# Kernel optimization log

Hardware: AMD Instinct MI355X
Metric: run time of the kernel (lower is better)

Reference implementation:

```python
import jax, jax.numpy as jnp
import numpy as np

NUM_HEADS = 32
NUM_KV_HEADS = 8
HEAD_DIM = 64
HIDDEN = 2048
EPS = 1e-05
ROPE_THETA = 1000000.0


def _rmsnorm(x, w):
    # x: [..., head_dim]
    var = jnp.mean(x * x, axis=-1, keepdims=True)
    return w * (x * jax.lax.rsqrt(var + EPS))


def _rope(q, k):
    # q,k: [B, h, T, d]
    T, d = q.shape[2], q.shape[3]
    inv_freq = 1.0 / (ROPE_THETA ** (jnp.arange(0, d, 2, dtype=jnp.float32) / d))
    t = jnp.arange(T, dtype=jnp.float32)
    freqs = jnp.outer(t, inv_freq)               # [T, d/2]
    emb = jnp.concatenate([freqs, freqs], -1)    # [T, d]
    cos = jnp.cos(emb)[None, None].astype(q.dtype)
    sin = jnp.sin(emb)[None, None].astype(q.dtype)

    def rotate(x):
        x1, x2 = x[..., : d // 2], x[..., d // 2 :]
        return jnp.concatenate([-x2, x1], -1)

    return q * cos + rotate(q) * sin, k * cos + rotate(k) * sin


def setup_inputs() -> dict:
    key = jax.random.key(0)
    ks = jax.random.split(key, 7)
    s = 0.02
    x = jax.random.normal(ks[0], (2, 2048, HIDDEN), jnp.float32)
    Wq = jax.random.normal(ks[1], (HIDDEN, NUM_HEADS * HEAD_DIM), jnp.float32) * s
    Wk = jax.random.normal(ks[2], (HIDDEN, NUM_KV_HEADS * HEAD_DIM), jnp.float32) * s
    Wv = jax.random.normal(ks[3], (HIDDEN, NUM_KV_HEADS * HEAD_DIM), jnp.float32) * s
    Wo = jax.random.normal(ks[4], (NUM_HEADS * HEAD_DIM, HIDDEN), jnp.float32) * s
    q_ln_w = jnp.ones((HEAD_DIM,), jnp.float32)
    k_ln_w = jnp.ones((HEAD_DIM,), jnp.float32)
    return {"x": x, "Wq": Wq, "Wk": Wk, "Wv": Wv, "Wo": Wo, "q_ln_w": q_ln_w, "k_ln_w": k_ln_w}


def reference(x, Wq, Wk, Wv, Wo, q_ln_w, k_ln_w):
    B, T, _ = x.shape
    g = NUM_HEADS // NUM_KV_HEADS  # GQA groups = 4
    q = (x @ Wq).reshape(B, T, NUM_HEADS, HEAD_DIM)
    k = (x @ Wk).reshape(B, T, NUM_KV_HEADS, HEAD_DIM)
    v = (x @ Wv).reshape(B, T, NUM_KV_HEADS, HEAD_DIM)
    q = _rmsnorm(q, q_ln_w)
    k = _rmsnorm(k, k_ln_w)
    q = q.transpose(0, 2, 1, 3)  # [B, nh, T, d]
    k = k.transpose(0, 2, 1, 3)  # [B, nkv, T, d]
    v = v.transpose(0, 2, 1, 3)
    q, k = _rope(q, k)
    # native GQA: fold query heads into (kv_head, group) without repeating K/V
    qg = q.reshape(B, NUM_KV_HEADS, g, T, HEAD_DIM)
    scale = 1.0 / jnp.sqrt(jnp.array(HEAD_DIM, q.dtype))
    scores = jnp.einsum("bkgtd,bksd->bkgts", qg, k) * scale  # [B,nkv,g,T,T]
    causal = jnp.tril(jnp.ones((T, T), bool))
    scores = jnp.where(causal, scores, jnp.finfo(scores.dtype).min)
    probs = jax.nn.softmax(scores, axis=-1)
    out = jnp.einsum("bkgts,bksd->bkgtd", probs, v)  # [B,nkv,g,T,d]
    out = out.reshape(B, NUM_HEADS, T, HEAD_DIM).transpose(0, 2, 1, 3).reshape(B, T, -1)
    return out @ Wo
```

## Files before the change

### kernel.cpp

```cpp
#include <hip/hip_runtime.h>
#include <cstdint>
#include <cstddef>

typedef unsigned short u16;
typedef __attribute__((ext_vector_type(8))) short short8;
typedef __attribute__((ext_vector_type(4))) short short4v;
typedef __attribute__((ext_vector_type(4))) float float4v;
typedef __attribute__((ext_vector_type(4))) unsigned short ushort4v;
typedef __attribute__((ext_vector_type(2))) float float2v;

__device__ __forceinline__ u16 f2bf(float f) {
    union { float f; uint32_t u; } x; x.f = f;
    uint32_t r = x.u + 0x7fffu + ((x.u >> 16) & 1u);
    return (u16)(r >> 16);
}
__device__ __forceinline__ uint32_t pack_bf16x2(float lo, float hi) {
    union { float f; uint32_t u; } a, b; a.f = lo; b.f = hi;
    return __builtin_amdgcn_perm(b.u + 0x8000u, a.u + 0x8000u, 0x07060302u);
}
__device__ __forceinline__ void gl_lds16(const u16* g, u16* l) {
    __builtin_amdgcn_global_load_lds(
        (const __attribute__((address_space(1))) void*)g,
        (__attribute__((address_space(3))) void*)l, 16, 0, 0);
}

__global__ __launch_bounds__(256) void prep(const float4v* __restrict__ x,
                                            const float* __restrict__ Wq,
                                            const float* __restrict__ Wk,
                                            const float* __restrict__ Wv,
                                            const float* __restrict__ Wo,
                                            ushort4v* __restrict__ xb,
                                            u16* __restrict__ wqkv_t,
                                            u16* __restrict__ wo_t,
                                            float2v* __restrict__ tab) {
    __shared__ float lds[64][33];
    const int bid = blockIdx.x;
    const int tid = threadIdx.x;
    if (bid < 8192) {
        const int i = bid * 256 + tid;
        float4v v = x[i];
        ushort4v o;
        #pragma unroll
        for (int j = 0; j < 4; ++j) o[j] = f2bf(v[j]);
        xb[i] = o;
        return;
    }
    if (bid < 8448) {
        const int idx = (bid - 8192) * 256 + tid;
        const int t = idx >> 5;
        const int i = idx & 31;
        const float invf = exp2f(-(float)i * (19.931568569324174f / 32.0f));
        float sv, cv;
        sincosf((float)t * invf, &sv, &cv);
        float2v o; o[0] = cv; o[1] = sv;
        tab[idx] = o;
        return;
    }
    const float* src;
    int Ns, n0, k0, scol0;
    u16* dst;
    if (bid < 11520) {
        const int id = bid - 8448;
        const int bx = id % 96, by = id / 96;
        n0 = bx * 32; k0 = by * 64;
        if (n0 < 2048)      { src = Wq; Ns = 2048; scol0 = n0; }
        else if (n0 < 2560) { src = Wk; Ns = 512;  scol0 = n0 - 2048; }
        else                { src = Wv; Ns = 512;  scol0 = n0 - 2560; }
        dst = wqkv_t;
    } else {
        const int id = bid - 11520;
        const int bx = id & 63, by = id >> 6;
        n0 = bx * 32; k0 = by * 64;
        src = Wo; Ns = 2048; scol0 = n0;
        dst = wo_t;
    }
    const int row64 = tid >> 2;
    const int c8    = (tid & 3) * 8;
    const float* sp = src + (size_t)(k0 + row64) * Ns + scol0 + c8;
    const float4v va = *(const float4v*)sp;
    const float4v vb = *(const float4v*)(sp + 4);
    #pragma unroll
    for (int i = 0; i < 4; ++i) { lds[row64][c8 + i] = va[i]; lds[row64][c8 + 4 + i] = vb[i]; }
    __syncthreads();
    const int nrow = tid >> 3;
    const int kk   = (tid & 7) * 8;
    short8 o8;
    #pragma unroll
    for (int i = 0; i < 8; ++i) o8[i] = (short)f2bf(lds[kk + i][nrow]);
    *(short8*)(dst + (size_t)(n0 + nrow) * 2048 + k0 + kk) = o8;
}

__global__ __launch_bounds__(256, 3) void gemm_bt(const u16* __restrict__ A,
                                                  const u16* __restrict__ Bt,
                                                  float* __restrict__ C,
                                                  int M, int N, int K) {
    __shared__ u16 lds_a[128 * 32];
    __shared__ u16 lds_b[128 * 32];
    const int tid  = threadIdx.x;
    const int wave = tid >> 6;
    const int lane = tid & 63;
    const int quad = lane >> 4;
    const int l15  = lane & 15;
    const long m0 = (long)blockIdx.x * 128;
    const long n0 = (long)blockIdx.y * 128;
    const int wm = (wave >> 1) * 64;
    const int wn = (wave & 1) * 64;
    const int s_row = tid >> 2;
    const int s_col = (tid & 3) * 8;

    float4v acc[4][4];
    #pragma unroll
    for (int i = 0; i < 4; ++i)
        #pragma unroll
        for (int j = 0; j < 4; ++j)
            #pragma unroll
            for (int r = 0; r < 4; ++r) acc[i][j][r] = 0.0f;

    const u16* ga0 = A  + (m0 + s_row) * (long)K + s_col;
    const u16* ga1 = ga0 + 64 * (long)K;
    const u16* gb0 = Bt + (n0 + s_row) * (long)K + s_col;
    const u16* gb1 = gb0 + 64 * (long)K;
    u16* la = lds_a + tid * 8;
    u16* lb = lds_b + tid * 8;

    const int n_k = K >> 5;
    for (int it = 0; it < n_k; ++it) {
        const int k0 = it << 5;
        gl_lds16(ga0 + k0, la);
        gl_lds16(ga1 + k0, la + 2048);
        gl_lds16(gb0 + k0, lb);
        gl_lds16(gb1 + k0, lb + 2048);
        __syncthreads();
        short8 af[4], bfr[4];
        #pragma unroll
        for (int mt = 0; mt < 4; ++mt)
            af[mt] = *(const short8*)(lds_a + (wm + mt * 16 + l15) * 32 + quad * 8);
        #pragma unroll
        for (int nt = 0; nt < 4; ++nt)
            bfr[nt] = *(const short8*)(lds_b + (wn + nt * 16 + l15) * 32 + quad * 8);
        #pragma unroll
        for (int mt = 0; mt < 4; ++mt)
            #pragma unroll
            for (int nt = 0; nt < 4; ++nt)
                acc[mt][nt] = __builtin_amdgcn_mfma_f32_16x16x32_bf16(af[mt], bfr[nt], acc[mt][nt], 0, 0, 0);
        __syncthreads();
    }
    #pragma unroll
    for (int mt = 0; mt < 4; ++mt) {
        #pragma unroll
        for (int nt = 0; nt < 4; ++nt) {
            const long gr = m0 + wm + mt * 16 + quad * 4;
            const long gc = n0 + wn + nt * 16 + l15;
            #pragma unroll
            for (int r = 0; r < 4; ++r)
                C[(gr + r) * N + gc] = acc[mt][nt][r];
        }
    }
}

__global__ __launch_bounds__(256, 3) void gemm_qkv(const u16* __restrict__ A,
                                                   const u16* __restrict__ Bt,
                                                   const float* __restrict__ qw,
                                                   const float* __restrict__ kw,
                                                   const float2v* __restrict__ tab,
                                                   u16* __restrict__ Qr,
                                                   u16* __restrict__ Kr,
                                                   u16* __restrict__ Vt) {
    const int K = 2048;
    __shared__ u16 lds_a[128 * 32];
    __shared__ u16 lds_b[128 * 32];
    const int tid  = threadIdx.x;
    const int wave = tid >> 6;
    const int lane = tid & 63;
    const int quad = lane >> 4;
    const int l15  = lane & 15;
    const long m0 = (long)blockIdx.x * 128;
    const long n0 = (long)blockIdx.y * 128;
    const int wm = (wave >> 1) * 64;
    const int wn = (wave & 1) * 64;
    const int s_row = tid >> 2;
    const int s_col = (tid & 3) * 8;

    float4v acc[4][4];
    #pragma unroll
    for (int i = 0; i < 4; ++i)
        #pragma unroll
        for (int j = 0; j < 4; ++j)
            #pragma unroll
            for (int r = 0; r < 4; ++r) acc[i][j][r] = 0.0f;

    const u16* ga0 = A  + (m0 + s_row) * (long)K + s_col;
    const u16* ga1 = ga0 + 64 * (long)K;
    const u16* gb0 = Bt + (n0 + s_row) * (long)K + s_col;
    const u16* gb1 = gb0 + 64 * (long)K;
    u16* la = lds_a + tid * 8;
    u16* lb = lds_b + tid * 8;

    const int n_k = K >> 5;
    for (int it = 0; it < n_k; ++it) {
        const int k0 = it << 5;
        gl_lds16(ga0 + k0, la);
        gl_lds16(ga1 + k0, la + 2048);
        gl_lds16(gb0 + k0, lb);
        gl_lds16(gb1 + k0, lb + 2048);
        __syncthreads();
        short8 af[4], bfr[4];
        #pragma unroll
        for (int mt = 0; mt < 4; ++mt)
            af[mt] = *(const short8*)(lds_a + (wm + mt * 16 + l15) * 32 + quad * 8);
        #pragma unroll
        for (int nt = 0; nt < 4; ++nt)
            bfr[nt] = *(const short8*)(lds_b + (wn + nt * 16 + l15) * 32 + quad * 8);
        #pragma unroll
        for (int mt = 0; mt < 4; ++mt)
            #pragma unroll
            for (int nt = 0; nt < 4; ++nt)
                acc[mt][nt] = __builtin_amdgcn_mfma_f32_16x16x32_bf16(af[mt], bfr[nt], acc[mt][nt], 0, 0, 0);
        __syncthreads();
    }

    const int col0 = (int)n0 + wn;
    if (col0 < 2560) {
        const bool isQ = (col0 < 2048);
        const float* lw = isQ ? qw : kw;
        float wreg[4];
        #pragma unroll
        for (int nt = 0; nt < 4; ++nt) wreg[nt] = lw[nt * 16 + l15];
        const float qs = isQ ? 0.18033688011112042f : 1.0f;
        const int swm = isQ ? 0 : 7;
        u16* dst = isQ ? (Qr + ((size_t)(col0 >> 6)) * 2048 * 64)
                       : (Kr + ((size_t)((col0 - 2048) >> 6)) * 2048 * 64);
        const size_t head_stride = isQ ? ((size_t)32 * 2048 * 64) : ((size_t)8 * 2048 * 64);
        #pragma unroll
        for (int mt = 0; mt < 4; ++mt) {
            const int gr0 = (int)m0 + wm + mt * 16 + quad * 4;
            const int b = gr0 >> 11, tt0 = gr0 & 2047;
            float rms[4];
            #pragma unroll
            for (int r = 0; r < 4; ++r) {
                float s = 0.0f;
                #pragma unroll
                for (int nt = 0; nt < 4; ++nt) s += acc[mt][nt][r] * acc[mt][nt][r];
                s += __shfl_xor(s, 1);
                s += __shfl_xor(s, 2);
                s += __shfl_xor(s, 4);
                s += __shfl_xor(s, 8);
                rms[r] = rsqrtf(s * (1.0f / 64.0f) + 1e-5f);
            }
            u16* rowp = dst + (size_t)b * head_stride + (size_t)tt0 * 64;
            #pragma unroll
            for (int nt = 0; nt < 2; ++nt) {
                const int i = nt * 16 + l15;
                #pragma unroll
                for (int r = 0; r < 4; ++r) {
                    const float2v cs = tab[(tt0 + r) * 32 + i];
                    const float v1 = acc[mt][nt][r]     * rms[r] * wreg[nt];
                    const float v2 = acc[mt][nt + 2][r] * rms[r] * wreg[nt + 2];
                    const float o1 = (v1 * cs[0] - v2 * cs[1]) * qs;
                    const float o2 = (v2 * cs[0] + v1 * cs[1]) * qs;
                    const int k7 = (tt0 + r) & swm;
                    const int i1 = (((i >> 3) ^ k7) << 3) | (i & 7);
                    const int i2 = ((((i + 32) >> 3) ^ k7) << 3) | (i & 7);
                    rowp[(size_t)r * 64 + i1] = f2bf(o1);
                    rowp[(size_t)r * 64 + i2] = f2bf(o2);
                }
            }
        }
    } else {
        const int kh = (col0 - 2560) >> 6;
        #pragma unroll
        for (int mt = 0; mt < 4; ++mt) {
            const int gr0 = (int)m0 + wm + mt * 16 + quad * 4;
            const int b = gr0 >> 11, tt0 = gr0 & 2047;
            const int tb = tt0 & ~63;
            const int tl = tt0 & 63;
            const int p0b = ((tl & 15) >> 2) * 16 + (tl >> 4) * 4;
            #pragma unroll
            for (int nt = 0; nt < 4; ++nt) {
                const int d = nt * 16 + l15;
                ushort4v o;
                #pragma unroll
                for (int r = 0; r < 4; ++r) o[r] = f2bf(acc[mt][nt][r]);
                const int col = tb + ((((p0b >> 3) ^ (d & 7)) << 3) | (p0b & 7));
                *(ushort4v*)(Vt + (((size_t)(b * 8 + kh)) * 64 + d) * 2048 + col) = o;
            }
        }
    }
}

#define SOFTMAX_PACK(S, l_i, pf)                                            \
    {                                                                       \
        float rs = 0.0f;                                                    \
        _Pragma("unroll")                                                   \
        for (int nt = 0; nt < 4; ++nt)                                      \
            _Pragma("unroll")                                               \
            for (int r = 0; r < 4; ++r) {                                   \
                const float pv = __builtin_amdgcn_exp2f(S[nt][r] - 12.0f);  \
                S[nt][r] = pv;                                              \
                rs += pv;                                                   \
            }                                                               \
        l_i += rs;                                                          \
        _Pragma("unroll")                                                   \
        for (int nt = 0; nt < 4; ++nt) {                                    \
            union { uint32_t u[2]; short4v s; } pu;                         \
            pu.u[0] = pack_bf16x2(S[nt][0], S[nt][1]);                      \
            pu.u[1] = pack_bf16x2(S[nt][2], S[nt][3]);                      \
            pf[nt] = pu.s;                                                  \
        }                                                                   \
    }

#define WRITE_O(O, l_i, qrow)                                               \
    {                                                                       \
        float lt = l_i;                                                     \
        lt += __shfl_xor(lt, 16);                                           \
        lt += __shfl_xor(lt, 32);                                           \
        const float rl = 1.0f / lt;                                         \
        _Pragma("unroll")                                                   \
        for (int dt = 0; dt < 4; ++dt) {                                    \
            ushort4v o;                                                     \
            _Pragma("unroll")                                               \
            for (int r = 0; r < 4; ++r) o[r] = f2bf(O[dt][r] * rl);         \
            *(ushort4v*)(Ob + ((size_t)(b * 2048 + (qrow))) * 2048 +        \
                         h * 64 + dt * 16 + quad * 4) = o;                  \
        }                                                                   \
    }

__global__ __launch_bounds__(256, 4) void attn_fwd(const u16* __restrict__ Qr,
                                                   const u16* __restrict__ Kr,
                                                   const u16* __restrict__ Vt,
                                                   u16* __restrict__ Ob) {
    __shared__ u16 lds_k[2][64 * 64];
    __shared__ u16 lds_v[2][64 * 64];
    const int tid  = threadIdx.x;
    const int wave = tid >> 6;
    const int lane = tid & 63;
    const int quad = lane >> 4;
    const int l15  = lane & 15;
    const int sw7  = l15 & 7;
    const int qx = 15 - blockIdx.y;
    const int bh = blockIdx.x;
    const int b = bh >> 5, h = bh & 31;
    const int kh = h >> 2;
    const u16* Qh = Qr + ((size_t)(b * 32 + h))  * 2048 * 64;
    const u16* Kh = Kr + ((size_t)(b * 8 + kh))  * 2048 * 64;
    const u16* Vh = Vt + ((size_t)(b * 8 + kh))  * 64 * 2048;

    const int qrow_c0 = qx * 128 + wave * 32 + l15;
    const int qrow_c1 = qrow_c0 + 16;
    short8 qf[2][2];
    #pragma unroll
    for (int ks = 0; ks < 2; ++ks) {
        qf[0][ks] = *(const short8*)(Qh + (size_t)qrow_c0 * 64 + ks * 32 + quad * 8);
        qf[1][ks] = *(const short8*)(Qh + (size_t)qrow_c1 * 64 + ks * 32 + quad * 8);
    }

    float l0v = 0.0f, l1v = 0.0f;
    float4v O0[4], O1[4];
    #pragma unroll
    for (int dt = 0; dt < 4; ++dt)
        #pragma unroll
        for (int r = 0; r < 4; ++r) { O0[dt][r] = 0.0f; O1[dt][r] = 0.0f; }

    const int vrow = tid >> 3;
    const int vchk = (tid & 7) * 8;
    auto stage = [&](int pb, int k0) {
        #pragma unroll
        for (int j = 0; j < 2; ++j)
            gl_lds16(Kh + (size_t)k0 * 64 + (j * 256 + tid) * 8,
                     &lds_k[pb][(j * 256 + tid) * 8]);
        #pragma unroll
        for (int j = 0; j < 2; ++j)
            gl_lds16(Vh + (size_t)(j * 32 + vrow) * 2048 + k0 + vchk,
                     &lds_v[pb][(j * 256 + tid) * 8]);
    };
    stage(0, 0);
    __syncthreads();

    const int n_it = 2 * qx + 2;
    for (int i = 0; i < n_it; ++i) {
        const int p = i & 1;
        const int kt0 = i << 6;

        if (i + 1 < n_it) stage(1 - p, (i + 1) << 6);

        float4v S0[4], S1[4];
        #pragma unroll
        for (int nt = 0; nt < 4; ++nt)
            #pragma unroll
            for (int r = 0; r < 4; ++r) { S0[nt][r] = 0.0f; S1[nt][r] = 0.0f; }
        __builtin_amdgcn_s_setprio(1);
        #pragma unroll
        for (int ks = 0; ks < 2; ++ks) {
            #pragma unroll
            for (int nt = 0; nt < 4; ++nt) {
                short8 kf = *(const short8*)(lds_k[p] + (nt * 16 + l15) * 64 +
                                             (((ks * 4 + quad) ^ sw7) << 3));
                S0[nt] = __builtin_amdgcn_mfma_f32_16x16x32_bf16(kf, qf[0][ks], S0[nt], 0, 0, 0);
                S1[nt] = __builtin_amdgcn_mfma_f32_16x16x32_bf16(kf, qf[1][ks], S1[nt], 0, 0, 0);
            }
        }
        __builtin_amdgcn_s_setprio(0);

        if (i >= n_it - 2) {
            #pragma unroll
            for (int nt = 0; nt < 4; ++nt) {
                const int keyb = kt0 + nt * 16 + quad * 4;
                #pragma unroll
                for (int r = 0; r < 4; ++r) {
                    if (keyb + r > qrow_c0) S0[nt][r] = -3e38f;
                    if (keyb + r > qrow_c1) S1[nt][r] = -3e38f;
                }
            }
        }

        short4v pf0[4], pf1[4];
        SOFTMAX_PACK(S0, l0v, pf0);
        SOFTMAX_PACK(S1, l1v, pf1);

        __builtin_amdgcn_s_setprio(1);
        #pragma unroll
        for (int nt2 = 0; nt2 < 2; ++nt2) {
            #pragma unroll
            for (int dt = 0; dt < 4; ++dt) {
                short8 vv = *(const short8*)(lds_v[p] + (dt * 16 + l15) * 64 +
                                             (((quad * 2 + nt2) ^ sw7) << 3));
                short4v vlo = __builtin_shufflevector(vv, vv, 0, 1, 2, 3);
                short4v vhi = __builtin_shufflevector(vv, vv, 4, 5, 6, 7);
                O0[dt] = __builtin_amdgcn_mfma_f32_16x16x16bf16_1k(vlo, pf0[2 * nt2],     O0[dt], 0, 0, 0);
                O0[dt] = __builtin_amdgcn_mfma_f32_16x16x16bf16_1k(vhi, pf0[2 * nt2 + 1], O0[dt], 0, 0, 0);
                O1[dt] = __builtin_amdgcn_mfma_f32_16x16x16bf16_1k(vlo, pf1[2 * nt2],     O1[dt], 0, 0, 0);
                O1[dt] = __builtin_amdgcn_mfma_f32_16x16x16bf16_1k(vhi, pf1[2 * nt2 + 1], O1[dt], 0, 0, 0);
            }
        }
        __builtin_amdgcn_s_setprio(0);

        __syncthreads();
    }
    WRITE_O(O0, l0v, qrow_c0);
    WRITE_O(O1, l1v, qrow_c1);
}

extern "C" void kernel_launch(void* const* d_in, const int* in_sizes, int n_in,
                              void* d_out, int out_size, void* d_ws, size_t ws_size,
                              hipStream_t stream) {
    (void)in_sizes; (void)n_in; (void)out_size; (void)ws_size;
    const float* x  = (const float*)d_in[0];
    const float* Wq = (const float*)d_in[1];
    const float* Wk = (const float*)d_in[2];
    const float* Wv = (const float*)d_in[3];
    const float* Wo = (const float*)d_in[4];
    const float* qw = (const float*)d_in[5];
    const float* kw = (const float*)d_in[6];
    float* out = (float*)d_out;

    char* ws = (char*)d_ws;
    size_t off = 0;
    auto alloc = [&](size_t bytes) {
        char* p = ws + off;
        off += (bytes + 255) & ~(size_t)255;
        return p;
    };
    u16* xb     = (u16*)alloc((size_t)8388608 * 2);
    u16* wqkv_t = (u16*)alloc((size_t)3072 * 2048 * 2);
    u16* wo_t   = (u16*)alloc((size_t)2048 * 2048 * 2);
    u16* q_r    = (u16*)alloc((size_t)2 * 32 * 2048 * 64 * 2);
    u16* k_r    = (u16*)alloc((size_t)2 * 8 * 2048 * 64 * 2);
    u16* v_r    = (u16*)alloc((size_t)2 * 8 * 64 * 2048 * 2);
    float2v* rtab = (float2v*)alloc((size_t)2048 * 32 * 8);
    u16* attnb  = xb;

    hipLaunchKernelGGL(prep, dim3(13568), dim3(256), 0, stream,
                       (const float4v*)x, Wq, Wk, Wv, Wo,
                       (ushort4v*)xb, wqkv_t, wo_t, rtab);
    hipLaunchKernelGGL(gemm_qkv, dim3(32, 24), dim3(256), 0, stream,
                       xb, wqkv_t, qw, kw, rtab, q_r, k_r, v_r);
    hipLaunchKernelGGL(attn_fwd, dim3(64, 16), dim3(256), 0, stream, q_r, k_r, v_r, attnb);
    hipLaunchKernelGGL(gemm_bt, dim3(32, 16), dim3(256), 0, stream,
                       attnb, wo_t, out, 4096, 2048, 2048);
}
```

Before: 279.0 us.

## Rewrite QKV GEMM as 256x256 tile with double-buffered ping-pong LDS pipeline

```diff
diff --git a/kernel.cpp b/kernel.cpp
--- a/kernel.cpp
+++ b/kernel.cpp
@@ -158,131 +158,206 @@
     }
 }
 
-__global__ __launch_bounds__(256, 3) void gemm_qkv(const u16* __restrict__ A,
-                                                   const u16* __restrict__ Bt,
-                                                   const float* __restrict__ qw,
-                                                   const float* __restrict__ kw,
-                                                   const float2v* __restrict__ tab,
-                                                   u16* __restrict__ Qr,
-                                                   u16* __restrict__ Kr,
-                                                   u16* __restrict__ Vt) {
-    const int K = 2048;
-    __shared__ u16 lds_a[128 * 32];
-    __shared__ u16 lds_b[128 * 32];
-    const int tid  = threadIdx.x;
+#define ACCL(mh, mt, nl) acc[mh][mt][(nl) >> 1][(nl) & 1]
+
+__device__ __forceinline__ void gemm256_pipe(const u16* __restrict__ A,
+                                             const u16* __restrict__ B,
+                                             const int K, const int nkt,
+                                             u16* lds, const int tid,
+                                             const long m0, const long n0,
+                                             float4v acc[2][4][2][2]) {
     const int wave = tid >> 6;
     const int lane = tid & 63;
     const int quad = lane >> 4;
     const int l15  = lane & 15;
-    const long m0 = (long)blockIdx.x * 128;
-    const long n0 = (long)blockIdx.y * 128;
-    const int wm = (wave >> 1) * 64;
-    const int wn = (wave & 1) * 64;
-    const int s_row = tid >> 2;
-    const int s_col = (tid & 3) * 8;
-
-    float4v acc[4][4];
-    #pragma unroll
-    for (int i = 0; i < 4; ++i)
-        #pragma unroll
-        for (int j = 0; j < 4; ++j)
-            #pragma unroll
-            for (int r = 0; r < 4; ++r) acc[i][j][r] = 0.0f;
-
-    const u16* ga0 = A  + (m0 + s_row) * (long)K + s_col;
-    const u16* ga1 = ga0 + 64 * (long)K;
-    const u16* gb0 = Bt + (n0 + s_row) * (long)K + s_col;
-    const u16* gb1 = gb0 + 64 * (long)K;
-    u16* la = lds_a + tid * 8;
-    u16* lb = lds_b + tid * 8;
-
-    const int n_k = K >> 5;
-    for (int it = 0; it < n_k; ++it) {
-        const int k0 = it << 5;
-        gl_lds16(ga0 + k0, la);
-        gl_lds16(ga1 + k0, la + 2048);
-        gl_lds16(gb0 + k0, lb);
-        gl_lds16(gb1 + k0, lb + 2048);
-        __syncthreads();
-        short8 af[4], bfr[4];
+    const int wr = wave >> 2;
+    const int wc = wave & 3;
+    const int sw7 = l15 & 7;
+
+    #pragma unroll
+    for (int a = 0; a < 2; ++a)
+        #pragma unroll
+        for (int b = 0; b < 4; ++b)
+            #pragma unroll
+            for (int c = 0; c < 2; ++c)
+                #pragma unroll
+                for (int d = 0; d < 2; ++d)
+                    #pragma unroll
+                    for (int r = 0; r < 4; ++r) acc[a][b][c][d][r] = 0.0f;
+
+    auto stg = [&](int kt, int type, int h) {
+        if (kt >= nkt) return;
+        u16* dst = lds + (kt & 1) * 32768 + type * 16384 + h * 8192;
+        const u16* src = type ? B : A;
+        const long r0 = (type ? n0 : m0) + h * 128;
+        const long k0 = (long)kt << 6;
+        #pragma unroll
+        for (int j = 0; j < 2; ++j) {
+            const int cid = tid + j * 512;
+            const int row = cid >> 3;
+            const int lc  = (cid & 7) ^ (row & 7);
+            gl_lds16(src + (r0 + row) * (long)K + k0 + lc * 8, dst + cid * 8);
+        }
+    };
+    short8 aA[4][2], bB0[2][2], bB1[2][2];
+    auto rdA = [&](int b, int mh) {
+        const u16* base = lds + b * 32768;
+        #pragma unroll
+        for (int mt = 0; mt < 4; ++mt) {
+            const int row = mh * 128 + wr * 64 + mt * 16 + l15;
+            #pragma unroll
+            for (int kk = 0; kk < 2; ++kk)
+                aA[mt][kk] = *(const short8*)(base + row * 64 + (((kk * 4 + quad) ^ sw7) << 3));
+        }
+    };
+    auto rdB = [&](int b, int nh, short8 (&bb)[2][2]) {
+        const u16* base = lds + b * 32768 + 16384;
+        #pragma unroll
+        for (int nt = 0; nt < 2; ++nt) {
+            const int row = wc * 64 + nh * 32 + nt * 16 + l15;
+            #pragma unroll
+            for (int kk = 0; kk < 2; ++kk)
+                bb[nt][kk] = *(const short8*)(base + row * 64 + (((kk * 4 + quad) ^ sw7) << 3));
+        }
+    };
+    auto mm = [&](int mh, int nh, short8 (&bb)[2][2]) {
+        __builtin_amdgcn_s_setprio(1);
         #pragma unroll
         for (int mt = 0; mt < 4; ++mt)
-            af[mt] = *(const short8*)(lds_a + (wm + mt * 16 + l15) * 32 + quad * 8);
-        #pragma unroll
-        for (int nt = 0; nt < 4; ++nt)
-            bfr[nt] = *(const short8*)(lds_b + (wn + nt * 16 + l15) * 32 + quad * 8);
-        #pragma unroll
-        for (int mt = 0; mt < 4; ++mt)
-            #pragma unroll
-            for (int nt = 0; nt < 4; ++nt)
-                acc[mt][nt] = __builtin_amdgcn_mfma_f32_16x16x32_bf16(af[mt], bfr[nt], acc[mt][nt], 0, 0, 0);
-        __syncthreads();
-    }
-
-    const int col0 = (int)n0 + wn;
+            #pragma unroll
+            for (int nt = 0; nt < 2; ++nt)
+                #pragma unroll
+                for (int kk = 0; kk < 2; ++kk)
+                    acc[mh][mt][nh][nt] = __builtin_amdgcn_mfma_f32_16x16x32_bf16(
+                        aA[mt][kk], bb[nt][kk], acc[mh][mt][nh][nt], 0, 0, 0);
+        __builtin_amdgcn_s_setprio(0);
+    };
+    #define GFENCE asm volatile("" ::: "memory")
+    #define GBAR() do { GFENCE; __builtin_amdgcn_s_barrier(); GFENCE; } while (0)
+    #define GLG0() do { asm volatile("s_waitcnt lgkmcnt(0)" ::: "memory"); \
+                        __builtin_amdgcn_sched_barrier(0); } while (0)
+
+    stg(0, 0, 0); stg(0, 1, 0); stg(0, 1, 1); stg(0, 0, 1);
+    stg(1, 0, 0); stg(1, 1, 0); stg(1, 1, 1);
+    asm volatile("s_waitcnt vmcnt(6)" ::: "memory");
+    GBAR();
+
+    for (int t = 0; t < nkt; t += 2) {
+        const bool lastIt = (t + 2 >= nkt);
+        rdA(0, 0); rdB(0, 0, bB0); stg(t + 1, 0, 1);
+        GBAR(); GLG0(); mm(0, 0, bB0); GBAR();
+        rdB(0, 1, bB1); stg(t + 2, 0, 0);
+        GBAR(); GLG0(); mm(0, 1, bB1); GBAR();
+        rdA(0, 1); stg(t + 2, 1, 0);
+        GBAR(); GLG0(); mm(1, 1, bB1); GBAR();
+        stg(t + 2, 1, 1);
+        if (lastIt) { asm volatile("s_waitcnt vmcnt(0)" ::: "memory"); }
+        else        { asm volatile("s_waitcnt vmcnt(6)" ::: "memory"); }
+        GBAR(); mm(1, 0, bB0); GBAR();
+        rdA(1, 0); rdB(1, 0, bB0); stg(t + 2, 0, 1);
+        GBAR(); GLG0(); mm(0, 0, bB0); GBAR();
+        rdB(1, 1, bB1); stg(t + 3, 0, 0);
+        GBAR(); GLG0(); mm(0, 1, bB1); GBAR();
+        rdA(1, 1); stg(t + 3, 1, 0);
+        GBAR(); GLG0(); mm(1, 1, bB1); GBAR();
+        stg(t + 3, 1, 1);
+        if (lastIt) { asm volatile("s_waitcnt vmcnt(0)" ::: "memory"); }
+        else        { asm volatile("s_waitcnt vmcnt(6)" ::: "memory"); }
+        GBAR(); mm(1, 0, bB0); GBAR();
+    }
+}
+
+__global__ __launch_bounds__(512) void gemm_qkv(const u16* __restrict__ A,
+                                                const u16* __restrict__ Bt,
+                                                const float* __restrict__ qw,
+                                                const float* __restrict__ kw,
+                                                const float2v* __restrict__ tab,
+                                                u16* __restrict__ Qr,
+                                                u16* __restrict__ Kr,
+                                                u16* __restrict__ Vt) {
+    __shared__ u16 lds[65536];
+    const int tid = threadIdx.x;
+    const int lane = tid & 63;
+    const int quad = lane >> 4;
+    const int l15  = lane & 15;
+    const int wr = (tid >> 6) >> 2;
+    const int wc = (tid >> 6) & 3;
+    const long m0 = (long)blockIdx.x * 256;
+    const long n0 = (long)blockIdx.y * 256;
+
+    float4v acc[2][4][2][2];
+    gemm256_pipe(A, Bt, 2048, 32, lds, tid, m0, n0, acc);
+
+    const int col0 = (int)n0 + wc * 64;
     if (col0 < 2560) {
         const bool isQ = (col0 < 2048);
         const float* lw = isQ ? qw : kw;
         float wreg[4];
         #pragma unroll
-        for (int nt = 0; nt < 4; ++nt) wreg[nt] = lw[nt * 16 + l15];
+        for (int nl = 0; nl < 4; ++nl) wreg[nl] = lw[nl * 16 + l15];
         const float qs = isQ ? 0.18033688011112042f : 1.0f;
         const int swm = isQ ? 0 : 7;
         u16* dst = isQ ? (Qr + ((size_t)(col0 >> 6)) * 2048 * 64)
                        : (Kr + ((size_t)((col0 - 2048) >> 6)) * 2048 * 64);
         const size_t head_stride = isQ ? ((size_t)32 * 2048 * 64) : ((size_t)8 * 2048 * 64);
         #pragma unroll
-        for (int mt = 0; mt < 4; ++mt) {
-            const int gr0 = (int)m0 + wm + mt * 16 + quad * 4;
-            const int b = gr0 >> 11, tt0 = gr0 & 2047;
-            float rms[4];
-            #pragma unroll
-            for (int r = 0; r < 4; ++r) {
-                float s = 0.0f;
-                #pragma unroll
-                for (int nt = 0; nt < 4; ++nt) s += acc[mt][nt][r] * acc[mt][nt][r];
-                s += __shfl_xor(s, 1);
-                s += __shfl_xor(s, 2);
-                s += __shfl_xor(s, 4);
-                s += __shfl_xor(s, 8);
-                rms[r] = rsqrtf(s * (1.0f / 64.0f) + 1e-5f);
-            }
-            u16* rowp = dst + (size_t)b * head_stride + (size_t)tt0 * 64;
-            #pragma unroll
-            for (int nt = 0; nt < 2; ++nt) {
-                const int i = nt * 16 + l15;
+        for (int mh = 0; mh < 2; ++mh) {
+            #pragma unroll
+            for (int mt = 0; mt < 4; ++mt) {
+                const int gr0 = (int)m0 + mh * 128 + wr * 64 + mt * 16 + quad * 4;
+                const int b = gr0 >> 11, tt0 = gr0 & 2047;
+                float rms[4];
                 #pragma unroll
                 for (int r = 0; r < 4; ++r) {
-                    const float2v cs = tab[(tt0 + r) * 32 + i];
-                    const float v1 = acc[mt][nt][r]     * rms[r] * wreg[nt];
-                    const float v2 = acc[mt][nt + 2][r] * rms[r] * wreg[nt + 2];
-                    const float o1 = (v1 * cs[0] - v2 * cs[1]) * qs;
-                    const float o2 = (v2 * cs[0] + v1 * cs[1]) * qs;
-                    const int k7 = (tt0 + r) & swm;
-                    const int i1 = (((i >> 3) ^ k7) << 3) | (i & 7);
-                    const int i2 = ((((i + 32) >> 3) ^ k7) << 3) | (i & 7);
-                    rowp[(size_t)r * 64 + i1] = f2bf(o1);
-                    rowp[(size_t)r * 64 + i2] = f2bf(o2);
+                    float s = 0.0f;
+                    #pragma unroll
+                    for (int nl = 0; nl < 4; ++nl) s += ACCL(mh, mt, nl)[r] * ACCL(mh, mt, nl)[r];
+                    s += __shfl_xor(s, 1);
+                    s += __shfl_xor(s, 2);
+                    s += __shfl_xor(s, 4);
+                    s += __shfl_xor(s, 8);
+                    rms[r] = rsqrtf(s * (1.0f / 64.0f) + 1e-5f);
+                }
+                u16* rowp = dst + (size_t)b * head_stride + (size_t)tt0 * 64;
+                #pragma unroll
+                for (int nl = 0; nl < 2; ++nl) {
+                    const int i = nl * 16 + l15;
+                    #pragma unroll
+                    for (int r = 0; r < 4; ++r) {
+                        const float2v cs = tab[(tt0 + r) * 32 + i];
+                        const float v1 = ACCL(mh, mt, nl)[r]     * rms[r] * wreg[nl];
+                        const float v2 = ACCL(mh, mt, nl + 2)[r] * rms[r] * wreg[nl + 2];
+                        const float o1 = (v1 * cs[0] - v2 * cs[1]) * qs;
+                        const float o2 = (v2 * cs[0] + v1 * cs[1]) * qs;
+                        const int k7 = (tt0 + r) & swm;
+                        const int i1 = (((i >> 3) ^ k7) << 3) | (i & 7);
+                        const int i2 = ((((i + 32) >> 3) ^ k7) << 3) | (i & 7);
+                        rowp[(size_t)r * 64 + i1] = f2bf(o1);
+                        rowp[(size_t)r * 64 + i2] = f2bf(o2);
+                    }
                 }
             }
         }
     } else {
         const int kh = (col0 - 2560) >> 6;
         #pragma unroll
-        for (int mt = 0; mt < 4; ++mt) {
-            const int gr0 = (int)m0 + wm + mt * 16 + quad * 4;
-            const int b = gr0 >> 11, tt0 = gr0 & 2047;
-            const int tb = tt0 & ~63;
-            const int tl = tt0 & 63;
-            const int p0b = ((tl & 15) >> 2) * 16 + (tl >> 4) * 4;
-            #pragma unroll
-            for (int nt = 0; nt < 4; ++nt) {
-                const int d = nt * 16 + l15;
-                ushort4v o;
+        for (int mh = 0; mh < 2; ++mh) {
+            #pragma unroll
+            for (int mt = 0; mt < 4; ++mt) {
+                const int gr0 = (int)m0 + mh * 128 + wr * 64 + mt * 16 + quad * 4;
+                const int b = gr0 >> 11, tt0 = gr0 & 2047;
+                const int tb = tt0 & ~63;
+                const int tl = tt0 & 63;
+                const int p0b = ((tl & 15) >> 2) * 16 + (tl >> 4) * 4;
                 #pragma unroll
-                for (int r = 0; r < 4; ++r) o[r] = f2bf(acc[mt][nt][r]);
-                const int col = tb + ((((p0b >> 3) ^ (d & 7)) << 3) | (p0b & 7));
-                *(ushort4v*)(Vt + (((size_t)(b * 8 + kh)) * 64 + d) * 2048 + col) = o;
+                for (int nl = 0; nl < 4; ++nl) {
+                    const int d = nl * 16 + l15;
+                    ushort4v o;
+                    #pragma unroll
+                    for (int r = 0; r < 4; ++r) o[r] = f2bf(ACCL(mh, mt, nl)[r]);
+                    const int col = tb + ((((p0b >> 3) ^ (d & 7)) << 3) | (p0b & 7));
+                    *(ushort4v*)(Vt + (((size_t)(b * 8 + kh)) * 64 + d) * 2048 + col) = o;
+                }
             }
         }
     }
@@ -472,7 +547,7 @@
     hipLaunchKernelGGL(prep, dim3(13568), dim3(256), 0, stream,
                        (const float4v*)x, Wq, Wk, Wv, Wo,
                        (ushort4v*)xb, wqkv_t, wo_t, rtab);
-    hipLaunchKernelGGL(gemm_qkv, dim3(32, 24), dim3(256), 0, stream,
+    hipLaunchKernelGGL(gemm_qkv, dim3(16, 12), dim3(512), 0, stream,
                        xb, wqkv_t, qw, kw, rtab, q_r, k_r, v_r);
     hipLaunchKernelGGL(attn_fwd, dim3(64, 16), dim3(256), 0, stream, q_r, k_r, v_r, attnb);
     hipLaunchKernelGGL(gemm_bt, dim3(32, 16), dim3(256), 0, stream,
```

New measurement: 278.3 us. About the same (-0.2%).

## Double-buffer LDS tiles in QKV and output GEMMs to prefetch next K-slice

Applied to the files above, without the earlier changes.

```diff
diff --git a/kernel.cpp b/kernel.cpp
--- a/kernel.cpp
+++ b/kernel.cpp
@@ -90,12 +90,13 @@
     *(short8*)(dst + (size_t)(n0 + nrow) * 2048 + k0 + kk) = o8;
 }
 
+
 __global__ __launch_bounds__(256, 3) void gemm_bt(const u16* __restrict__ A,
                                                   const u16* __restrict__ Bt,
                                                   float* __restrict__ C,
                                                   int M, int N, int K) {
-    __shared__ u16 lds_a[128 * 32];
-    __shared__ u16 lds_b[128 * 32];
+    __shared__ u16 lds_a[2][128 * 32];
+    __shared__ u16 lds_b[2][128 * 32];
     const int tid  = threadIdx.x;
     const int wave = tid >> 6;
     const int lane = tid & 63;
@@ -120,24 +121,30 @@
     const u16* ga1 = ga0 + 64 * (long)K;
     const u16* gb0 = Bt + (n0 + s_row) * (long)K + s_col;
     const u16* gb1 = gb0 + 64 * (long)K;
-    u16* la = lds_a + tid * 8;
-    u16* lb = lds_b + tid * 8;
-
+
+    auto stg = [&](int buf, int it) {
+        const int k0 = it << 5;
+        u16* La = lds_a[buf] + tid * 8;
+        u16* Lb = lds_b[buf] + tid * 8;
+        gl_lds16(ga0 + k0, La);
+        gl_lds16(ga1 + k0, La + 2048);
+        gl_lds16(gb0 + k0, Lb);
+        gl_lds16(gb1 + k0, Lb + 2048);
+    };
+
+    stg(0, 0);
+    __syncthreads();
     const int n_k = K >> 5;
     for (int it = 0; it < n_k; ++it) {
-        const int k0 = it << 5;
-        gl_lds16(ga0 + k0, la);
-        gl_lds16(ga1 + k0, la + 2048);
-        gl_lds16(gb0 + k0, lb);
-        gl_lds16(gb1 + k0, lb + 2048);
-        __syncthreads();
+        const int p = it & 1;
+        if (it + 1 < n_k) stg(1 - p, it + 1);
         short8 af[4], bfr[4];
         #pragma unroll
         for (int mt = 0; mt < 4; ++mt)
-            af[mt] = *(const short8*)(lds_a + (wm + mt * 16 + l15) * 32 + quad * 8);
+            af[mt] = *(const short8*)(lds_a[p] + (wm + mt * 16 + l15) * 32 + quad * 8);
         #pragma unroll
         for (int nt = 0; nt < 4; ++nt)
-            bfr[nt] = *(const short8*)(lds_b + (wn + nt * 16 + l15) * 32 + quad * 8);
+            bfr[nt] = *(const short8*)(lds_b[p] + (wn + nt * 16 + l15) * 32 + quad * 8);
         #pragma unroll
         for (int mt = 0; mt < 4; ++mt)
             #pragma unroll
@@ -167,8 +174,8 @@
                                                    u16* __restrict__ Kr,
                                                    u16* __restrict__ Vt) {
     const int K = 2048;
-    __shared__ u16 lds_a[128 * 32];
-    __shared__ u16 lds_b[128 * 32];
+    __shared__ u16 lds_a[2][128 * 32];
+    __shared__ u16 lds_b[2][128 * 32];
     const int tid  = threadIdx.x;
     const int wave = tid >> 6;
     const int lane = tid & 63;
@@ -193,24 +200,30 @@
     const u16* ga1 = ga0 + 64 * (long)K;
     const u16* gb0 = Bt + (n0 + s_row) * (long)K + s_col;
     const u16* gb1 = gb0 + 64 * (long)K;
-    u16* la = lds_a + tid * 8;
-    u16* lb = lds_b + tid * 8;
-
+
+    auto stg = [&](int buf, int it) {
+        const int k0 = it << 5;
+        u16* La = lds_a[buf] + tid * 8;
+        u16* Lb = lds_b[buf] + tid * 8;
+        gl_lds16(ga0 + k0, La);
+        gl_lds16(ga1 + k0, La + 2048);
+        gl_lds16(gb0 + k0, Lb);
+        gl_lds16(gb1 + k0, Lb + 2048);
+    };
+
+    stg(0, 0);
+    __syncthreads();
     const int n_k = K >> 5;
     for (int it = 0; it < n_k; ++it) {
-        const int k0 = it << 5;
-        gl_lds16(ga0 + k0, la);
-        gl_lds16(ga1 + k0, la + 2048);
-        gl_lds16(gb0 + k0, lb);
-        gl_lds16(gb1 + k0, lb + 2048);
-        __syncthreads();
+        const int p = it & 1;
+        if (it + 1 < n_k) stg(1 - p, it + 1);
         short8 af[4], bfr[4];
         #pragma unroll
         for (int mt = 0; mt < 4; ++mt)
-            af[mt] = *(const short8*)(lds_a + (wm + mt * 16 + l15) * 32 + quad * 8);
+            af[mt] = *(const short8*)(lds_a[p] + (wm + mt * 16 + l15) * 32 + quad * 8);
         #pragma unroll
         for (int nt = 0; nt < 4; ++nt)
-            bfr[nt] = *(const short8*)(lds_b + (wn + nt * 16 + l15) * 32 + quad * 8);
+            bfr[nt] = *(const short8*)(lds_b[p] + (wn + nt * 16 + l15) * 32 + quad * 8);
         #pragma unroll
         for (int mt = 0; mt < 4; ++mt)
             #pragma unroll
```

Result: slower. 285.0 us (+2.2%).
